# Optimization experiments

Measured on AMD Instinct MI355X. Metric: run time of the kernel, lower is better.

## Reference

```python
import jax, jax.numpy as jnp
import numpy as np

B, N, D = 8, 2048, 128

def setup_inputs() -> dict:
    key = jax.random.key(0)
    k1, k2, k3 = jax.random.split(key, 3)
    h = jax.random.normal(k1, (B, N, D), dtype=jnp.float32)
    W = jax.random.normal(k2, (D, D), dtype=jnp.float32) * (1.0 / np.sqrt(D))
    # a has shape [1,1,1,2D] in torch; flatten to [2D] (xavier-normal init)
    a = jax.random.normal(k3, (2 * D,), dtype=jnp.float32) * np.sqrt(2.0 / (2 * D))
    return {"h": h, "W": W, "a": a}

def reference(h, W, a):
    act = jax.nn.relu
    # h <- h @ W^T (nn.Linear with weight W means x @ W.T; here W is the weight matrix)
    hw = jnp.einsum('bnd,ed->bne', h, W)  # [B,N,D]
    a_i, a_j = a[:D], a[D:]
    # e_ij = act(a_i . h_i + a_j . h_j) -- equivalent to sum(cat(h_i,h_j)*a, -1)
    s_i = jnp.einsum('bnd,d->bn', hw, a_i)  # [B,N]
    s_j = jnp.einsum('bnd,d->bn', hw, a_j)  # [B,N]
    e = act(s_i[:, :, None] + s_j[:, None, :])  # [B,N,N]
    a_ij = jax.nn.softmax(e, axis=2)
    out = act(jnp.einsum('bij,bjd->bid', a_ij, hw))
    return out
```

## Files before the change

### kernel.cpp

```cpp
#include <hip/hip_runtime.h>
#include <hip/hip_bf16.h>

#define BB 8
#define NN 2048
#define DD 128
#define TI 32
#define HP 132
#define CH 32
#define NC (NN / CH)
#define NO (NC + 1)
#define NFIX (BB * NO)

__device__ __forceinline__ float relu(float x) { return x > 0.f ? x : 0.f; }

__global__ __launch_bounds__(256) void GraphAttentionalLayer_1168231104632_tr(
    const float* __restrict__ W, float* __restrict__ WT)
{
    const int g = blockIdx.x * 256 + threadIdx.x;
    const int d = g >> 7, e = g & 127;
    WT[g] = W[e * DD + d];
}

__global__ __launch_bounds__(256) void GraphAttentionalLayer_1168231104632_kernel(
    const float* __restrict__ h,
    const float* __restrict__ WT,
    const float* __restrict__ a,
    float* __restrict__ hw,
    float* __restrict__ E,
    float* __restrict__ F)
{
    __shared__ float h_s[TI][HP];
    __shared__ float wt_s[32][HP];

    const int tid = threadIdx.x;
    const int t = tid & 127;
    const int hh = tid >> 7;
    const int tx = tid & 31, ty = tid >> 5;
    const int b = blockIdx.x >> 6;
    const int i0 = (blockIdx.x & 63) * TI;
    const size_t base = ((size_t)b * NN + i0) * DD;

    for (int r = hh; r < TI; r += 2)
        h_s[r][t] = h[base + (size_t)r * DD + t];

    const int e0 = tx * 4, r0 = ty * 4;
    float acc[4][4];
#pragma unroll
    for (int i = 0; i < 4; i++)
#pragma unroll
        for (int j = 0; j < 4; j++) acc[i][j] = 0.f;

    for (int dc = 0; dc < DD; dc += 32) {
        __syncthreads();
        for (int rr = hh; rr < 32; rr += 2)
            wt_s[rr][t] = WT[(size_t)(dc + rr) * DD + t];
        __syncthreads();
#pragma unroll 4
        for (int dd = 0; dd < 32; dd++) {
            const float4 wv = *reinterpret_cast<const float4*>(&wt_s[dd][e0]);
            const float w4[4] = {wv.x, wv.y, wv.z, wv.w};
#pragma unroll
            for (int r = 0; r < 4; r++) {
                const float hv = h_s[r0 + r][dc + dd];
#pragma unroll
                for (int e = 0; e < 4; e++) acc[r][e] += hv * w4[e];
            }
        }
    }

#pragma unroll
    for (int r = 0; r < 4; r++) {
        float4 o = make_float4(acc[r][0], acc[r][1], acc[r][2], acc[r][3]);
        *reinterpret_cast<float4*>(&hw[base + (size_t)(r0 + r) * DD + e0]) = o;
    }

    const float4 aiv = *reinterpret_cast<const float4*>(&a[e0]);
    const float4 ajv = *reinterpret_cast<const float4*>(&a[DD + e0]);
    const float ai4[4] = {aiv.x, aiv.y, aiv.z, aiv.w};
    const float aj4[4] = {ajv.x, ajv.y, ajv.z, ajv.w};
#pragma unroll
    for (int r = 0; r < 4; r++) {
        float pi = 0.f, pj = 0.f;
#pragma unroll
        for (int e = 0; e < 4; e++) { pi += acc[r][e] * ai4[e]; pj += acc[r][e] * aj4[e]; }
#pragma unroll
        for (int off = 16; off > 0; off >>= 1) {
            pi += __shfl_down(pi, off, 32);
            pj += __shfl_down(pj, off, 32);
        }
        if (tx == 0) {
            const size_t row = (size_t)b * NN + i0 + r0 + r;
            E[row] = __expf(pi);
            F[row] = __expf(pj);
        }
    }
}

__global__ __launch_bounds__(256) void GraphAttentionalLayer_1168231104632_rank(
    const float* __restrict__ F,
    float* __restrict__ Fsorted,
    int* __restrict__ perm)
{
    __shared__ float F_s[NN];
    __shared__ int   part[4][64];

    const int t = threadIdx.x;
    const int b = blockIdx.x >> 5;
    const int j0 = (blockIdx.x & 31) * 64;
    const size_t nb = (size_t)b * NN;

    for (int q = 0; q < NN / 256; q++)
        F_s[q * 256 + t] = F[nb + q * 256 + t];
    __syncthreads();

    const int tj = t & 63, ts = t >> 6;
    const int j = j0 + tj;
    const float fj = F_s[j];
    const int m0 = ts * (NN / 4);
    int cnt = 0;
#pragma unroll 8
    for (int mi = 0; mi < NN / 4; mi++) {
        const int m = m0 + mi;
        const float fm = F_s[m];
        cnt += (fm < fj) | ((fm == fj) & (m < j));
    }
    part[ts][tj] = cnt;
    __syncthreads();
    if (ts == 0) {
        const int r = part[0][tj] + part[1][tj] + part[2][tj] + part[3][tj];
        Fsorted[nb + r] = fj;
        perm[nb + r] = j;
    }
}

__global__ __launch_bounds__(128) void GraphAttentionalLayer_1168231104632_scan(
    const float* __restrict__ hw,
    const float* __restrict__ Fsorted,
    const int* __restrict__ perm,
    float* __restrict__ Q0L, float* __restrict__ Q1L,
    float* __restrict__ C0,  float* __restrict__ C1)
{
    const int t = threadIdx.x;
    const int b = blockIdx.x / NC, c = blockIdx.x % NC;
    const size_t nb = (size_t)b * NN;
    const int m0 = c * CH;

    int   jv[CH];
    float Fv[CH];
#pragma unroll
    for (int mm = 0; mm < CH; mm++) jv[mm] = perm[nb + m0 + mm];
#pragma unroll
    for (int mm = 0; mm < CH; mm++) Fv[mm] = Fsorted[nb + m0 + mm];

    float hv[CH];
#pragma unroll
    for (int mm = 0; mm < CH; mm++)
        hv[mm] = hw[(nb + jv[mm]) * DD + t];

    float a0 = 0.f, a1 = 0.f;
#pragma unroll
    for (int mm = 0; mm < CH; mm++) {
        const int m = m0 + mm;
        Q0L[(nb + m) * DD + t] = a0;
        Q1L[(nb + m) * DD + t] = a1;
        a0 += hv[mm];
        a1 += Fv[mm] * hv[mm];
    }
    C0[((size_t)b * NC + c) * DD + t] = a0;
    C1[((size_t)b * NC + c) * DD + t] = a1;
}

__global__ __launch_bounds__(256) void GraphAttentionalLayer_1168231104632_mid(
    const float* __restrict__ C0, const float* __restrict__ C1,
    const float* __restrict__ Fsorted, const float* __restrict__ E,
    float* __restrict__ O0, float* __restrict__ O1,
    int* __restrict__ kk,  float* __restrict__ zinv)
{
    __shared__ float fs_s[NN];
    __shared__ float cf_s[NC];
    __shared__ float of_s[NO];

    const int tid = threadIdx.x;

    if (blockIdx.x < NFIX) {
        const int b = blockIdx.x / NO, c = blockIdx.x % NO;
        const int d = tid & 127;
        const float* C = (tid < 128) ? C0 : C1;
        float*       O = (tid < 128) ? O0 : O1;
        float o = 0.f;
        int c2 = 0;
        for (; c2 + 16 <= c; c2 += 16) {
            float v[16];
#pragma unroll
            for (int q = 0; q < 16; q++)
                v[q] = C[((size_t)b * NC + c2 + q) * DD + d];
#pragma unroll
            for (int q = 0; q < 16; q++) o += v[q];
        }
        for (; c2 < c; c2++)
            o += C[((size_t)b * NC + c2) * DD + d];
        O[((size_t)b * NO + c) * DD + d] = o;
        return;
    }

    const int sb = blockIdx.x - NFIX;
    const int b = sb >> 3;
    const int i0 = (sb & 7) * 256;
    const size_t nb = (size_t)b * NN;

    for (int q = 0; q < NN / 256; q++)
        fs_s[q * 256 + tid] = Fsorted[nb + q * 256 + tid];
    __syncthreads();

    if (tid < NC) {
        float p = 0.f;
        const int m0 = tid * CH;
#pragma unroll
        for (int mm = 0; mm < CH; mm++) p += fs_s[m0 + mm];
        cf_s[tid] = p;
    }
    __syncthreads();
    if (tid < NO) {
        float p = 0.f;
        for (int c2 = 0; c2 < tid; c2++) p += cf_s[c2];
        of_s[tid] = p;
    }
    __syncthreads();

    const int row = (int)nb + i0 + tid;
    const float Ei = E[row];
    const float thr = 1.0f / Ei;
    int lo = 0, hi = NN;
    while (lo < hi) {
        const int mid = (lo + hi) >> 1;
        if (fs_s[mid] < thr) lo = mid + 1; else hi = mid;
    }
    float fpl = 0.f;
    for (int m = (lo >> 5) << 5; m < lo; m++) fpl += fs_s[m];
    const float TF = of_s[NC];
    const float Pk = of_s[lo >> 5] + fpl;
    const float z = Ei * (TF - Pk) + (float)lo;
    kk[row] = lo;
    zinv[row] = 1.0f / z;
}

__global__ __launch_bounds__(128) void GraphAttentionalLayer_1168231104632_out(
    const float* __restrict__ Q0L, const float* __restrict__ Q1L,
    const float* __restrict__ O0,  const float* __restrict__ O1,
    const int* __restrict__ kk,    const float* __restrict__ zinv,
    const float* __restrict__ E,   float* __restrict__ out)
{
    const int t = threadIdx.x;
    const int row = blockIdx.x;
    const int b = row >> 11;
    const size_t nb = (size_t)b * NN;

    const int k = kk[row];
    const float Ev = E[row];
    const float zv = zinv[row];
    const float T1 = O1[((size_t)b * NO + NC) * DD + t];

    float num;
    if (k < NN) {
        const int c = k >> 5;
        const float q0 = Q0L[(nb + k) * DD + t] + O0[((size_t)b * NO + c) * DD + t];
        const float q1 = Q1L[(nb + k) * DD + t] + O1[((size_t)b * NO + c) * DD + t];
        num = Ev * (T1 - q1) + q0;
    } else {
        num = O0[((size_t)b * NO + NC) * DD + t];
    }
    out[(size_t)row * DD + t] = relu(num * zv);
}

extern "C" __attribute__((visibility("default")))
void kernel_launch(void* const* d_in, const int* in_sizes, int n_in,
                   void* d_out, int out_size, void* d_ws, size_t ws_size,
                   hipStream_t stream) {
    const float* h = nullptr; const float* W = nullptr; const float* a = nullptr;
    for (int i = 0; i < n_in; i++) {
        if (in_sizes[i] == BB * NN * DD)      h = (const float*)d_in[i];
        else if (in_sizes[i] == DD * DD)      W = (const float*)d_in[i];
        else if (in_sizes[i] == 2 * DD)       a = (const float*)d_in[i];
    }
    if (!h) h = (const float*)d_in[0];
    if (!W) W = (const float*)d_in[1];
    if (!a) a = (const float*)d_in[2];

    float* out = (float*)d_out;
    float* ws = (float*)d_ws;

    float* WT   = ws;
    float* hw   = WT + DD * DD;
    float* E    = hw + (size_t)BB * NN * DD;
    float* F    = E + BB * NN;
    float* Fs   = F + BB * NN;
    float* zinv = Fs + BB * NN;
    int*   perm = (int*)(zinv + BB * NN);
    int*   kk   = perm + BB * NN;
    float* Q0L  = (float*)(kk + BB * NN);
    float* Q1L  = Q0L + (size_t)BB * NN * DD;
    float* C0   = Q1L + (size_t)BB * NN * DD;
    float* C1   = C0 + BB * NC * DD;
    float* O0   = C1 + BB * NC * DD;
    float* O1   = O0 + BB * NO * DD;
    const size_t need = (size_t)((O1 + BB * NO * DD) - ws) * sizeof(float);

    if (ws_size < need || d_ws == nullptr) {
        hipMemsetAsync(d_out, 0x42, (size_t)out_size * sizeof(float), stream);
        return;
    }

    GraphAttentionalLayer_1168231104632_tr<<<(DD * DD) / 256, 256, 0, stream>>>(W, WT);
    GraphAttentionalLayer_1168231104632_kernel<<<BB * (NN / TI), 256, 0, stream>>>(h, WT, a, hw, E, F);
    GraphAttentionalLayer_1168231104632_rank<<<BB * 32, 256, 0, stream>>>(F, Fs, perm);
    GraphAttentionalLayer_1168231104632_scan<<<BB * NC, 128, 0, stream>>>(hw, Fs, perm, Q0L, Q1L, C0, C1);
    GraphAttentionalLayer_1168231104632_mid<<<NFIX + BB * 8, 256, 0, stream>>>(C0, C1, Fs, E, O0, O1, kk, zinv);
    GraphAttentionalLayer_1168231104632_out<<<BB * NN, 128, 0, stream>>>(Q0L, Q1L, O0, O1, kk, zinv, E, out);
}
```

Baseline: 112.7 us.

## Drop per-row prefix arrays; recompute intra-chunk partial sums in output kernel

The scan kernel no longer writes the full per-row prefix arrays Q0L/Q1L (two B*N*D float buffers) and now only emits per-chunk totals. The output kernel recomputes the within-chunk partial sums by gathering up to 31 rows of hw through the sorted permutation, split across two half-blocks and reduced in shared memory. It also remaps block order to interleave batches. The GEMM inner loop is rewritten to load h as float4 and process four d-steps per iteration, which reduces LDS instruction count. This trades heavy global writes and reads for extra gather reads, and per-row work now varies with the chunk remainder.

```diff
diff --git a/kernel.cpp b/kernel.cpp
--- a/kernel.cpp
+++ b/kernel.cpp
@@ -55,16 +55,27 @@
         for (int rr = hh; rr < 32; rr += 2)
             wt_s[rr][t] = WT[(size_t)(dc + rr) * DD + t];
         __syncthreads();
-#pragma unroll 4
-        for (int dd = 0; dd < 32; dd++) {
-            const float4 wv = *reinterpret_cast<const float4*>(&wt_s[dd][e0]);
-            const float w4[4] = {wv.x, wv.y, wv.z, wv.w};
+#pragma unroll
+        for (int dd = 0; dd < 32; dd += 4) {
+            float wq[4][4], hq[4][4];
+#pragma unroll
+            for (int q = 0; q < 4; q++) {
+                const float4 v = *reinterpret_cast<const float4*>(&wt_s[dd + q][e0]);
+                wq[q][0] = v.x; wq[q][1] = v.y; wq[q][2] = v.z; wq[q][3] = v.w;
+            }
 #pragma unroll
             for (int r = 0; r < 4; r++) {
-                const float hv = h_s[r0 + r][dc + dd];
-#pragma unroll
-                for (int e = 0; e < 4; e++) acc[r][e] += hv * w4[e];
+                const float4 v = *reinterpret_cast<const float4*>(&h_s[r0 + r][dc + dd]);
+                hq[r][0] = v.x; hq[r][1] = v.y; hq[r][2] = v.z; hq[r][3] = v.w;
             }
+#pragma unroll
+            for (int r = 0; r < 4; r++)
+#pragma unroll
+                for (int q = 0; q < 4; q++) {
+                    const float hv = hq[r][q];
+#pragma unroll
+                    for (int e = 0; e < 4; e++) acc[r][e] += hv * wq[q][e];
+                }
         }
     }
 
@@ -133,11 +144,10 @@
     }
 }
 
-__global__ __launch_bounds__(128) void GraphAttentionalLayer_1168231104632_scan(
+__global__ __launch_bounds__(128) void GraphAttentionalLayer_1168231104632_csum(
     const float* __restrict__ hw,
     const float* __restrict__ Fsorted,
     const int* __restrict__ perm,
-    float* __restrict__ Q0L, float* __restrict__ Q1L,
     float* __restrict__ C0,  float* __restrict__ C1)
 {
     const int t = threadIdx.x;
@@ -160,9 +170,6 @@
     float a0 = 0.f, a1 = 0.f;
 #pragma unroll
     for (int mm = 0; mm < CH; mm++) {
-        const int m = m0 + mm;
-        Q0L[(nb + m) * DD + t] = a0;
-        Q1L[(nb + m) * DD + t] = a1;
         a0 += hv[mm];
         a1 += Fv[mm] * hv[mm];
     }
@@ -244,32 +251,56 @@
     zinv[row] = 1.0f / z;
 }
 
-__global__ __launch_bounds__(128) void GraphAttentionalLayer_1168231104632_out(
-    const float* __restrict__ Q0L, const float* __restrict__ Q1L,
-    const float* __restrict__ O0,  const float* __restrict__ O1,
-    const int* __restrict__ kk,    const float* __restrict__ zinv,
-    const float* __restrict__ E,   float* __restrict__ out)
-{
-    const int t = threadIdx.x;
-    const int row = blockIdx.x;
+__global__ __launch_bounds__(256) void GraphAttentionalLayer_1168231104632_out(
+    const float* __restrict__ hw,
+    const int* __restrict__ perm, const float* __restrict__ Fsorted,
+    const float* __restrict__ O0, const float* __restrict__ O1,
+    const int* __restrict__ kk,   const float* __restrict__ zinv,
+    const float* __restrict__ E,  float* __restrict__ out)
+{
+    __shared__ int   pm_s[CH];
+    __shared__ float fj_s[CH];
+    __shared__ float q_s[2][2][DD];
+
+    const int tid = threadIdx.x;
+    const int t = tid & 127;
+    const int g = tid >> 7;
+    const int blk = blockIdx.x;
+    const int row = ((blk & 7) << 11) | (blk >> 3);
     const int b = row >> 11;
     const size_t nb = (size_t)b * NN;
 
     const int k = kk[row];
-    const float Ev = E[row];
-    const float zv = zinv[row];
-    const float T1 = O1[((size_t)b * NO + NC) * DD + t];
-
-    float num;
-    if (k < NN) {
-        const int c = k >> 5;
-        const float q0 = Q0L[(nb + k) * DD + t] + O0[((size_t)b * NO + c) * DD + t];
-        const float q1 = Q1L[(nb + k) * DD + t] + O1[((size_t)b * NO + c) * DD + t];
-        num = Ev * (T1 - q1) + q0;
-    } else {
-        num = O0[((size_t)b * NO + NC) * DD + t];
-    }
-    out[(size_t)row * DD + t] = relu(num * zv);
+    const int c = k >> 5;
+    const int rem = k & 31;
+
+    if (tid < CH && rem) {
+        pm_s[tid] = perm[nb + c * CH + tid];
+        fj_s[tid] = Fsorted[nb + c * CH + tid];
+    }
+    __syncthreads();
+
+    float q0 = 0.f, q1 = 0.f;
+#pragma unroll 4
+    for (int m = g; m < rem; m += 2) {
+        const int j = pm_s[m];
+        const float hv = hw[(nb + j) * DD + t];
+        q0 += hv;
+        q1 += fj_s[m] * hv;
+    }
+    q_s[0][g][t] = q0;
+    q_s[1][g][t] = q1;
+    __syncthreads();
+
+    if (tid < DD) {
+        const float Ev = E[row];
+        const float zv = zinv[row];
+        const float T1 = O1[((size_t)b * NO + NC) * DD + t];
+        const float Q0 = O0[((size_t)b * NO + c) * DD + t] + q_s[0][0][t] + q_s[0][1][t];
+        const float Q1 = O1[((size_t)b * NO + c) * DD + t] + q_s[1][0][t] + q_s[1][1][t];
+        const float num = Ev * (T1 - Q1) + Q0;
+        out[(size_t)row * DD + t] = relu(num * zv);
+    }
 }
 
 extern "C" __attribute__((visibility("default")))
@@ -297,9 +328,7 @@
     float* zinv = Fs + BB * NN;
     int*   perm = (int*)(zinv + BB * NN);
     int*   kk   = perm + BB * NN;
-    float* Q0L  = (float*)(kk + BB * NN);
-    float* Q1L  = Q0L + (size_t)BB * NN * DD;
-    float* C0   = Q1L + (size_t)BB * NN * DD;
+    float* C0   = (float*)(kk + BB * NN);
     float* C1   = C0 + BB * NC * DD;
     float* O0   = C1 + BB * NC * DD;
     float* O1   = O0 + BB * NO * DD;
@@ -313,7 +342,7 @@
     GraphAttentionalLayer_1168231104632_tr<<<(DD * DD) / 256, 256, 0, stream>>>(W, WT);
     GraphAttentionalLayer_1168231104632_kernel<<<BB * (NN / TI), 256, 0, stream>>>(h, WT, a, hw, E, F);
     GraphAttentionalLayer_1168231104632_rank<<<BB * 32, 256, 0, stream>>>(F, Fs, perm);
-    GraphAttentionalLayer_1168231104632_scan<<<BB * NC, 128, 0, stream>>>(hw, Fs, perm, Q0L, Q1L, C0, C1);
+    GraphAttentionalLayer_1168231104632_csum<<<BB * NC, 128, 0, stream>>>(hw, Fs, perm, C0, C1);
     GraphAttentionalLayer_1168231104632_mid<<<NFIX + BB * 8, 256, 0, stream>>>(C0, C1, Fs, E, O0, O1, kk, zinv);
-    GraphAttentionalLayer_1168231104632_out<<<BB * NN, 128, 0, stream>>>(Q0L, Q1L, O0, O1, kk, zinv, E, out);
-}
+    GraphAttentionalLayer_1168231104632_out<<<BB * NN, 256, 0, stream>>>(hw, perm, Fs, O0, O1, kk, zinv, E, out);
+}
```

Result: slower. 121.9 us (+8.1%).

## Fuse six stage kernels into one persistent kernel with grid barriers

Applied to the files above, without the earlier changes.

Replaces the six separate launches (transpose, projection, rank, scan, prefix, output) with one 512-block persistent kernel. Stages are separated by atomic-counter grid barriers, and a memset resets the counters before launch. The work per stage is redistributed to fit 512 blocks, for example rank uses 32 columns per block with 8 partial slices and output handles 32 rows per block. This removes the launch gaps and tail effects between kernels. In exchange it requires all 512 blocks to be co-resident and adds barrier spin costs.

```diff
diff --git a/kernel.cpp b/kernel.cpp
--- a/kernel.cpp
+++ b/kernel.cpp
@@ -10,266 +10,281 @@
 #define NC (NN / CH)
 #define NO (NC + 1)
 #define NFIX (BB * NO)
+#define GRID 512
+#define TPB 256
 
 __device__ __forceinline__ float relu(float x) { return x > 0.f ? x : 0.f; }
 
-__global__ __launch_bounds__(256) void GraphAttentionalLayer_1168231104632_tr(
-    const float* __restrict__ W, float* __restrict__ WT)
-{
-    const int g = blockIdx.x * 256 + threadIdx.x;
-    const int d = g >> 7, e = g & 127;
-    WT[g] = W[e * DD + d];
+__device__ __forceinline__ void gridbar(unsigned* bar, int p) {
+    __syncthreads();
+    if (threadIdx.x == 0) {
+        __threadfence();
+        __hip_atomic_fetch_add(&bar[p], 1u, __ATOMIC_ACQ_REL, __HIP_MEMORY_SCOPE_AGENT);
+        while (__hip_atomic_load(&bar[p], __ATOMIC_ACQUIRE, __HIP_MEMORY_SCOPE_AGENT) < GRID)
+            __builtin_amdgcn_s_sleep(1);
+        __threadfence();
+    }
+    __syncthreads();
 }
 
-__global__ __launch_bounds__(256) void GraphAttentionalLayer_1168231104632_kernel(
+__global__ __launch_bounds__(TPB, 2) void GraphAttentionalLayer_1168231104632_mega(
     const float* __restrict__ h,
-    const float* __restrict__ WT,
+    const float* __restrict__ W,
     const float* __restrict__ a,
-    float* __restrict__ hw,
-    float* __restrict__ E,
-    float* __restrict__ F)
+    float* __restrict__ out,
+    float* __restrict__ WT,  float* __restrict__ hw,
+    float* __restrict__ E,   float* __restrict__ F,
+    float* __restrict__ Fs,  float* __restrict__ zinv,
+    int* __restrict__ perm,  int* __restrict__ kk,
+    float* __restrict__ Q0L, float* __restrict__ Q1L,
+    float* __restrict__ C0,  float* __restrict__ C1,
+    float* __restrict__ O0,  float* __restrict__ O1,
+    unsigned* __restrict__ bar)
 {
     __shared__ float h_s[TI][HP];
     __shared__ float wt_s[32][HP];
-
-    const int tid = threadIdx.x;
-    const int t = tid & 127;
-    const int hh = tid >> 7;
-    const int tx = tid & 31, ty = tid >> 5;
-    const int b = blockIdx.x >> 6;
-    const int i0 = (blockIdx.x & 63) * TI;
-    const size_t base = ((size_t)b * NN + i0) * DD;
-
-    for (int r = hh; r < TI; r += 2)
-        h_s[r][t] = h[base + (size_t)r * DD + t];
-
-    const int e0 = tx * 4, r0 = ty * 4;
-    float acc[4][4];
-#pragma unroll
-    for (int i = 0; i < 4; i++)
-#pragma unroll
-        for (int j = 0; j < 4; j++) acc[i][j] = 0.f;
-
-    for (int dc = 0; dc < DD; dc += 32) {
-        __syncthreads();
-        for (int rr = hh; rr < 32; rr += 2)
-            wt_s[rr][t] = WT[(size_t)(dc + rr) * DD + t];
-        __syncthreads();
-#pragma unroll 4
-        for (int dd = 0; dd < 32; dd++) {
-            const float4 wv = *reinterpret_cast<const float4*>(&wt_s[dd][e0]);
-            const float w4[4] = {wv.x, wv.y, wv.z, wv.w};
-#pragma unroll
-            for (int r = 0; r < 4; r++) {
-                const float hv = h_s[r0 + r][dc + dd];
-#pragma unroll
-                for (int e = 0; e < 4; e++) acc[r][e] += hv * w4[e];
-            }
-        }
-    }
-
-#pragma unroll
-    for (int r = 0; r < 4; r++) {
-        float4 o = make_float4(acc[r][0], acc[r][1], acc[r][2], acc[r][3]);
-        *reinterpret_cast<float4*>(&hw[base + (size_t)(r0 + r) * DD + e0]) = o;
-    }
-
-    const float4 aiv = *reinterpret_cast<const float4*>(&a[e0]);
-    const float4 ajv = *reinterpret_cast<const float4*>(&a[DD + e0]);
-    const float ai4[4] = {aiv.x, aiv.y, aiv.z, aiv.w};
-    const float aj4[4] = {ajv.x, ajv.y, ajv.z, ajv.w};
-#pragma unroll
-    for (int r = 0; r < 4; r++) {
-        float pi = 0.f, pj = 0.f;
-#pragma unroll
-        for (int e = 0; e < 4; e++) { pi += acc[r][e] * ai4[e]; pj += acc[r][e] * aj4[e]; }
-#pragma unroll
-        for (int off = 16; off > 0; off >>= 1) {
-            pi += __shfl_down(pi, off, 32);
-            pj += __shfl_down(pj, off, 32);
-        }
-        if (tx == 0) {
-            const size_t row = (size_t)b * NN + i0 + r0 + r;
-            E[row] = __expf(pi);
-            F[row] = __expf(pj);
-        }
-    }
-}
-
-__global__ __launch_bounds__(256) void GraphAttentionalLayer_1168231104632_rank(
-    const float* __restrict__ F,
-    float* __restrict__ Fsorted,
-    int* __restrict__ perm)
-{
     __shared__ float F_s[NN];
-    __shared__ int   part[4][64];
-
-    const int t = threadIdx.x;
-    const int b = blockIdx.x >> 5;
-    const int j0 = (blockIdx.x & 31) * 64;
-    const size_t nb = (size_t)b * NN;
-
-    for (int q = 0; q < NN / 256; q++)
-        F_s[q * 256 + t] = F[nb + q * 256 + t];
-    __syncthreads();
-
-    const int tj = t & 63, ts = t >> 6;
-    const int j = j0 + tj;
-    const float fj = F_s[j];
-    const int m0 = ts * (NN / 4);
-    int cnt = 0;
-#pragma unroll 8
-    for (int mi = 0; mi < NN / 4; mi++) {
-        const int m = m0 + mi;
-        const float fm = F_s[m];
-        cnt += (fm < fj) | ((fm == fj) & (m < j));
-    }
-    part[ts][tj] = cnt;
-    __syncthreads();
-    if (ts == 0) {
-        const int r = part[0][tj] + part[1][tj] + part[2][tj] + part[3][tj];
-        Fsorted[nb + r] = fj;
-        perm[nb + r] = j;
-    }
-}
-
-__global__ __launch_bounds__(128) void GraphAttentionalLayer_1168231104632_scan(
-    const float* __restrict__ hw,
-    const float* __restrict__ Fsorted,
-    const int* __restrict__ perm,
-    float* __restrict__ Q0L, float* __restrict__ Q1L,
-    float* __restrict__ C0,  float* __restrict__ C1)
-{
-    const int t = threadIdx.x;
-    const int b = blockIdx.x / NC, c = blockIdx.x % NC;
-    const size_t nb = (size_t)b * NN;
-    const int m0 = c * CH;
-
-    int   jv[CH];
-    float Fv[CH];
-#pragma unroll
-    for (int mm = 0; mm < CH; mm++) jv[mm] = perm[nb + m0 + mm];
-#pragma unroll
-    for (int mm = 0; mm < CH; mm++) Fv[mm] = Fsorted[nb + m0 + mm];
-
-    float hv[CH];
-#pragma unroll
-    for (int mm = 0; mm < CH; mm++)
-        hv[mm] = hw[(nb + jv[mm]) * DD + t];
-
-    float a0 = 0.f, a1 = 0.f;
-#pragma unroll
-    for (int mm = 0; mm < CH; mm++) {
-        const int m = m0 + mm;
-        Q0L[(nb + m) * DD + t] = a0;
-        Q1L[(nb + m) * DD + t] = a1;
-        a0 += hv[mm];
-        a1 += Fv[mm] * hv[mm];
-    }
-    C0[((size_t)b * NC + c) * DD + t] = a0;
-    C1[((size_t)b * NC + c) * DD + t] = a1;
-}
-
-__global__ __launch_bounds__(256) void GraphAttentionalLayer_1168231104632_mid(
-    const float* __restrict__ C0, const float* __restrict__ C1,
-    const float* __restrict__ Fsorted, const float* __restrict__ E,
-    float* __restrict__ O0, float* __restrict__ O1,
-    int* __restrict__ kk,  float* __restrict__ zinv)
-{
-    __shared__ float fs_s[NN];
+    __shared__ int   part[8][32];
     __shared__ float cf_s[NC];
     __shared__ float of_s[NO];
+    __shared__ float T0s[DD], T1s[DD];
 
     const int tid = threadIdx.x;
-
-    if (blockIdx.x < NFIX) {
-        const int b = blockIdx.x / NO, c = blockIdx.x % NO;
-        const int d = tid & 127;
-        const float* C = (tid < 128) ? C0 : C1;
-        float*       O = (tid < 128) ? O0 : O1;
-        float o = 0.f;
-        int c2 = 0;
-        for (; c2 + 16 <= c; c2 += 16) {
-            float v[16];
-#pragma unroll
-            for (int q = 0; q < 16; q++)
-                v[q] = C[((size_t)b * NC + c2 + q) * DD + d];
-#pragma unroll
-            for (int q = 0; q < 16; q++) o += v[q];
-        }
-        for (; c2 < c; c2++)
-            o += C[((size_t)b * NC + c2) * DD + d];
-        O[((size_t)b * NO + c) * DD + d] = o;
-        return;
-    }
-
-    const int sb = blockIdx.x - NFIX;
-    const int b = sb >> 3;
-    const int i0 = (sb & 7) * 256;
-    const size_t nb = (size_t)b * NN;
-
-    for (int q = 0; q < NN / 256; q++)
-        fs_s[q * 256 + tid] = Fsorted[nb + q * 256 + tid];
-    __syncthreads();
-
-    if (tid < NC) {
-        float p = 0.f;
-        const int m0 = tid * CH;
-#pragma unroll
-        for (int mm = 0; mm < CH; mm++) p += fs_s[m0 + mm];
-        cf_s[tid] = p;
-    }
-    __syncthreads();
-    if (tid < NO) {
-        float p = 0.f;
-        for (int c2 = 0; c2 < tid; c2++) p += cf_s[c2];
-        of_s[tid] = p;
-    }
-    __syncthreads();
-
-    const int row = (int)nb + i0 + tid;
-    const float Ei = E[row];
-    const float thr = 1.0f / Ei;
-    int lo = 0, hi = NN;
-    while (lo < hi) {
-        const int mid = (lo + hi) >> 1;
-        if (fs_s[mid] < thr) lo = mid + 1; else hi = mid;
-    }
-    float fpl = 0.f;
-    for (int m = (lo >> 5) << 5; m < lo; m++) fpl += fs_s[m];
-    const float TF = of_s[NC];
-    const float Pk = of_s[lo >> 5] + fpl;
-    const float z = Ei * (TF - Pk) + (float)lo;
-    kk[row] = lo;
-    zinv[row] = 1.0f / z;
-}
-
-__global__ __launch_bounds__(128) void GraphAttentionalLayer_1168231104632_out(
-    const float* __restrict__ Q0L, const float* __restrict__ Q1L,
-    const float* __restrict__ O0,  const float* __restrict__ O1,
-    const int* __restrict__ kk,    const float* __restrict__ zinv,
-    const float* __restrict__ E,   float* __restrict__ out)
-{
-    const int t = threadIdx.x;
-    const int row = blockIdx.x;
-    const int b = row >> 11;
-    const size_t nb = (size_t)b * NN;
-
-    const int k = kk[row];
-    const float Ev = E[row];
-    const float zv = zinv[row];
-    const float T1 = O1[((size_t)b * NO + NC) * DD + t];
-
-    float num;
-    if (k < NN) {
-        const int c = k >> 5;
-        const float q0 = Q0L[(nb + k) * DD + t] + O0[((size_t)b * NO + c) * DD + t];
-        const float q1 = Q1L[(nb + k) * DD + t] + O1[((size_t)b * NO + c) * DD + t];
-        num = Ev * (T1 - q1) + q0;
-    } else {
-        num = O0[((size_t)b * NO + NC) * DD + t];
-    }
-    out[(size_t)row * DD + t] = relu(num * zv);
+    const int blk = blockIdx.x;
+
+    {
+        const int g = blk * TPB + tid;
+        if (g < DD * DD) {
+            const int d = g >> 7, e = g & 127;
+            WT[g] = W[e * DD + d];
+        }
+    }
+    gridbar(bar, 0);
+
+    {
+        const int t = tid & 127;
+        const int hh = tid >> 7;
+        const int tx = tid & 31, ty = tid >> 5;
+        const int b = blk >> 6;
+        const int i0 = (blk & 63) * TI;
+        const size_t base = ((size_t)b * NN + i0) * DD;
+
+        for (int r = hh; r < TI; r += 2)
+            h_s[r][t] = h[base + (size_t)r * DD + t];
+
+        const int e0 = tx * 4, r0 = ty * 4;
+        float acc[4][4];
+#pragma unroll
+        for (int i = 0; i < 4; i++)
+#pragma unroll
+            for (int j = 0; j < 4; j++) acc[i][j] = 0.f;
+
+        for (int dc = 0; dc < DD; dc += 32) {
+            __syncthreads();
+            for (int rr = hh; rr < 32; rr += 2)
+                wt_s[rr][t] = WT[(size_t)(dc + rr) * DD + t];
+            __syncthreads();
+#pragma unroll 4
+            for (int dd = 0; dd < 32; dd++) {
+                const float4 wv = *reinterpret_cast<const float4*>(&wt_s[dd][e0]);
+                const float w4[4] = {wv.x, wv.y, wv.z, wv.w};
+#pragma unroll
+                for (int r = 0; r < 4; r++) {
+                    const float hv = h_s[r0 + r][dc + dd];
+#pragma unroll
+                    for (int e = 0; e < 4; e++) acc[r][e] += hv * w4[e];
+                }
+            }
+        }
+
+#pragma unroll
+        for (int r = 0; r < 4; r++) {
+            float4 o = make_float4(acc[r][0], acc[r][1], acc[r][2], acc[r][3]);
+            *reinterpret_cast<float4*>(&hw[base + (size_t)(r0 + r) * DD + e0]) = o;
+        }
+
+        const float4 aiv = *reinterpret_cast<const float4*>(&a[e0]);
+        const float4 ajv = *reinterpret_cast<const float4*>(&a[DD + e0]);
+        const float ai4[4] = {aiv.x, aiv.y, aiv.z, aiv.w};
+        const float aj4[4] = {ajv.x, ajv.y, ajv.z, ajv.w};
+#pragma unroll
+        for (int r = 0; r < 4; r++) {
+            float pi = 0.f, pj = 0.f;
+#pragma unroll
+            for (int e = 0; e < 4; e++) { pi += acc[r][e] * ai4[e]; pj += acc[r][e] * aj4[e]; }
+#pragma unroll
+            for (int off = 16; off > 0; off >>= 1) {
+                pi += __shfl_down(pi, off, 32);
+                pj += __shfl_down(pj, off, 32);
+            }
+            if (tx == 0) {
+                const size_t row = (size_t)b * NN + i0 + r0 + r;
+                E[row] = __expf(pi);
+                F[row] = __expf(pj);
+            }
+        }
+    }
+    gridbar(bar, 1);
+
+    {
+        const int b = blk >> 6;
+        const int j0 = (blk & 63) * 32;
+        const size_t nb = (size_t)b * NN;
+
+        for (int q = 0; q < NN / TPB; q++)
+            F_s[q * TPB + tid] = F[nb + q * TPB + tid];
+        __syncthreads();
+
+        const int tj = tid & 31, ts = tid >> 5;
+        const int j = j0 + tj;
+        const float fj = F_s[j];
+        const int m0 = ts * (NN / 8);
+        int cnt = 0;
+#pragma unroll 8
+        for (int mi = 0; mi < NN / 8; mi++) {
+            const int m = m0 + mi;
+            const float fm = F_s[m];
+            cnt += (fm < fj) | ((fm == fj) & (m < j));
+        }
+        part[ts][tj] = cnt;
+        __syncthreads();
+        if (ts == 0) {
+            int r = 0;
+#pragma unroll
+            for (int s = 0; s < 8; s++) r += part[s][tj];
+            Fs[nb + r] = fj;
+            perm[nb + r] = j;
+        }
+    }
+    gridbar(bar, 2);
+
+    if (tid < 128) {
+        const int t = tid;
+        const int b = blk >> 6, c = blk & 63;
+        const size_t nb = (size_t)b * NN;
+        const int m0 = c * CH;
+
+        int   jv[CH];
+        float Fv[CH];
+#pragma unroll
+        for (int mm = 0; mm < CH; mm++) jv[mm] = perm[nb + m0 + mm];
+#pragma unroll
+        for (int mm = 0; mm < CH; mm++) Fv[mm] = Fs[nb + m0 + mm];
+
+        float hv[CH];
+#pragma unroll
+        for (int mm = 0; mm < CH; mm++)
+            hv[mm] = hw[(nb + jv[mm]) * DD + t];
+
+        float a0 = 0.f, a1 = 0.f;
+#pragma unroll
+        for (int mm = 0; mm < CH; mm++) {
+            const int m = m0 + mm;
+            Q0L[(nb + m) * DD + t] = a0;
+            Q1L[(nb + m) * DD + t] = a1;
+            a0 += hv[mm];
+            a1 += Fv[mm] * hv[mm];
+        }
+        C0[((size_t)b * NC + c) * DD + t] = a0;
+        C1[((size_t)b * NC + c) * DD + t] = a1;
+    }
+    gridbar(bar, 3);
+
+    {
+        for (int idx = blk; idx < NFIX; idx += GRID) {
+            const int b = idx / NO, c = idx % NO;
+            const int d = tid & 127;
+            const float* C = (tid < 128) ? C0 : C1;
+            float*       O = (tid < 128) ? O0 : O1;
+            float o = 0.f;
+            int c2 = 0;
+            for (; c2 + 16 <= c; c2 += 16) {
+                float v[16];
+#pragma unroll
+                for (int q = 0; q < 16; q++)
+                    v[q] = C[((size_t)b * NC + c2 + q) * DD + d];
+#pragma unroll
+                for (int q = 0; q < 16; q++) o += v[q];
+            }
+            for (; c2 < c; c2++)
+                o += C[((size_t)b * NC + c2) * DD + d];
+            O[((size_t)b * NO + c) * DD + d] = o;
+        }
+
+        if (blk < BB * 8) {
+            const int b = blk >> 3;
+            const int i0 = (blk & 7) * 256;
+            const size_t nb = (size_t)b * NN;
+
+            __syncthreads();
+            for (int q = 0; q < NN / TPB; q++)
+                F_s[q * TPB + tid] = Fs[nb + q * TPB + tid];
+            __syncthreads();
+
+            if (tid < NC) {
+                float p = 0.f;
+                const int m0 = tid * CH;
+#pragma unroll
+                for (int mm = 0; mm < CH; mm++) p += F_s[m0 + mm];
+                cf_s[tid] = p;
+            }
+            __syncthreads();
+            if (tid < NO) {
+                float p = 0.f;
+                for (int c2 = 0; c2 < tid; c2++) p += cf_s[c2];
+                of_s[tid] = p;
+            }
+            __syncthreads();
+
+            const int row = (int)nb + i0 + tid;
+            const float Ei = E[row];
+            const float thr = 1.0f / Ei;
+            int lo = 0, hi = NN;
+            while (lo < hi) {
+                const int mid = (lo + hi) >> 1;
+                if (F_s[mid] < thr) lo = mid + 1; else hi = mid;
+            }
+            float fpl = 0.f;
+            for (int m = (lo >> 5) << 5; m < lo; m++) fpl += F_s[m];
+            const float TF = of_s[NC];
+            const float Pk = of_s[lo >> 5] + fpl;
+            const float z = Ei * (TF - Pk) + (float)lo;
+            kk[row] = lo;
+            zinv[row] = 1.0f / z;
+        }
+    }
+    gridbar(bar, 4);
+
+    {
+        const int t = tid & 127;
+        const int g = tid >> 7;
+        const int b = blk >> 6;
+        const int rb = (blk & 63) * 32;
+        const size_t nb = (size_t)b * NN;
+
+        if (tid < DD) {
+            T0s[tid] = O0[((size_t)b * NO + NC) * DD + tid];
+            T1s[tid] = O1[((size_t)b * NO + NC) * DD + tid];
+        }
+        __syncthreads();
+
+        for (int it = 0; it < 16; it++) {
+            const int row = (int)nb + rb + it * 2 + g;
+            const int k = kk[row];
+            const float Ev = E[row];
+            const float zv = zinv[row];
+            float num;
+            if (k < NN) {
+                const int c = k >> 5;
+                const float q0 = Q0L[(nb + k) * DD + t] + O0[((size_t)b * NO + c) * DD + t];
+                const float q1 = Q1L[(nb + k) * DD + t] + O1[((size_t)b * NO + c) * DD + t];
+                num = Ev * (T1s[t] - q1) + q0;
+            } else {
+                num = T0s[t];
+            }
+            out[(size_t)row * DD + t] = relu(num * zv);
+        }
+    }
 }
 
 extern "C" __attribute__((visibility("default")))
@@ -303,17 +318,17 @@
     float* C1   = C0 + BB * NC * DD;
     float* O0   = C1 + BB * NC * DD;
     float* O1   = O0 + BB * NO * DD;
-    const size_t need = (size_t)((O1 + BB * NO * DD) - ws) * sizeof(float);
+    unsigned* bar = (unsigned*)(O1 + BB * NO * DD);
+    const size_t need = ((char*)(bar + 16) - (char*)ws);
 
     if (ws_size < need || d_ws == nullptr) {
         hipMemsetAsync(d_out, 0x42, (size_t)out_size * sizeof(float), stream);
         return;
     }
 
-    GraphAttentionalLayer_1168231104632_tr<<<(DD * DD) / 256, 256, 0, stream>>>(W, WT);
-    GraphAttentionalLayer_1168231104632_kernel<<<BB * (NN / TI), 256, 0, stream>>>(h, WT, a, hw, E, F);
-    GraphAttentionalLayer_1168231104632_rank<<<BB * 32, 256, 0, stream>>>(F, Fs, perm);
-    GraphAttentionalLayer_1168231104632_scan<<<BB * NC, 128, 0, stream>>>(hw, Fs, perm, Q0L, Q1L, C0, C1);
-    GraphAttentionalLayer_1168231104632_mid<<<NFIX + BB * 8, 256, 0, stream>>>(C0, C1, Fs, E, O0, O1, kk, zinv);
-    GraphAttentionalLayer_1168231104632_out<<<BB * NN, 128, 0, stream>>>(Q0L, Q1L, O0, O1, kk, zinv, E, out);
+    hipMemsetAsync(bar, 0, 64, stream);
+    GraphAttentionalLayer_1168231104632_mega<<<GRID, TPB, 0, stream>>>(
+        h, W, a, out,
+        WT, hw, E, F, Fs, zinv, perm, kk,
+        Q0L, Q1L, C0, C1, O0, O1, bar);
 }
```

Result: slower. 376.6 us (+234.0%).
